# Performance work log

Measured on AMD Instinct MI355X. Metric: run time of the kernel, lower is better.

The kernel has to match this reference:

```python
import jax, jax.numpy as jnp
import numpy as np

N, E, G, H = 4096, 8192, 64, 128  # nodes, edges, graphs, hidden dim
NODE_DIM, EDGE_DIM = 11, 5


def _linear_params(key, fan_in, fan_out):
    kw, kb = jax.random.split(key)
    s = 1.0 / np.sqrt(fan_in)
    w = jax.random.uniform(kw, (fan_in, fan_out), minval=-s, maxval=s, dtype=jnp.float32)
    b = jax.random.uniform(kb, (fan_out,), minval=-s, maxval=s, dtype=jnp.float32)
    return w, b


def setup_inputs() -> dict:
    key = jax.random.key(0)
    ks = jax.random.split(key, 10)
    x = jax.random.normal(ks[0], (N, NODE_DIM), dtype=jnp.float32)
    edge_attr = jax.random.normal(ks[1], (E, EDGE_DIM), dtype=jnp.float32)
    edge_index = jax.random.randint(ks[2], (2, E), 0, N, dtype=jnp.int64)
    batch = jnp.sort(jax.random.randint(ks[3], (N,), 0, G, dtype=jnp.int64))
    # preprocess MLP: node_dim -> 128 -> 128
    p1_w, p1_b = _linear_params(ks[4], NODE_DIM, H)
    p2_w, p2_b = _linear_params(ks[5], H, H)
    # edge net: edge_dim -> 128 -> 256 -> 128 -> 128*128 (ReLU between, none after last)
    e1_w, e1_b = _linear_params(ks[6], EDGE_DIM, 128)
    e2_w, e2_b = _linear_params(ks[7], 128, 256)
    e3_w, e3_b = _linear_params(ks[8], 256, 128)
    e4_w, e4_b = _linear_params(ks[9], 128, H * H)
    return {"x": x, "edge_attr": edge_attr, "edge_index": edge_index, "batch": batch,
            "p1_w": p1_w, "p1_b": p1_b, "p2_w": p2_w, "p2_b": p2_b,
            "e1_w": e1_w, "e1_b": e1_b, "e2_w": e2_w, "e2_b": e2_b,
            "e3_w": e3_w, "e3_b": e3_b, "e4_w": e4_w, "e4_b": e4_b}


def reference(x, edge_attr, edge_index, batch,
              p1_w, p1_b, p2_w, p2_b,
              e1_w, e1_b, e2_w, e2_b, e3_w, e3_b, e4_w, e4_b):
    # node preprocess MLP (maps 11-dim features to 128 so NNConv dims are consistent)
    h = jax.nn.relu(x @ p1_w + p1_b) @ p2_w + p2_b  # [N, H]
    # edge network -> per-edge weight matrix [E, H, H]
    e = jax.nn.relu(edge_attr @ e1_w + e1_b)
    e = jax.nn.relu(e @ e2_w + e2_b)
    e = jax.nn.relu(e @ e3_w + e3_b)
    W = (e @ e4_w + e4_b).reshape(E, H, H)
    # NNConv (root_weight=False, bias=False, aggr='mean'):
    src, dst = edge_index[0], edge_index[1]
    msg = jnp.einsum('ei,eio->eo', h[src], W)  # gather + per-edge matmul, [E, H]
    agg = jax.ops.segment_sum(msg, dst, num_segments=N)
    cnt = jax.ops.segment_sum(jnp.ones((E,), msg.dtype), dst, num_segments=N)
    h_out = agg / jnp.maximum(cnt, 1.0)[:, None]  # scatter-mean, [N, H]
    # global add pool over graphs
    pooled = jax.ops.segment_sum(h_out, batch, num_segments=G)  # [G, H]
    return pooled
```

## Files before the change

kernel.cpp:

```cpp
#include <hip/hip_runtime.h>
#include <hip/hip_bf16.h>

#define N_NODES 4096
#define N_EDGES 8192
#define N_GRAPHS 64
#define HDIM 128

typedef __attribute__((ext_vector_type(8))) short bf16x8;
typedef __attribute__((ext_vector_type(4))) float f32x4;
typedef __attribute__((ext_vector_type(4))) unsigned short u16x4;

static __device__ __forceinline__ unsigned short f2bf(float f) {
    unsigned u = __builtin_bit_cast(unsigned, f);
    u += 0x7fffu + ((u >> 16) & 1u);
    return (unsigned short)(u >> 16);
}
static __device__ __forceinline__ float bf2f(unsigned short s) {
    unsigned u = ((unsigned)s) << 16;
    return __builtin_bit_cast(float, u);
}

__global__ __launch_bounds__(256) void fused_pre_kernel(
    const float* __restrict__ x, const float* __restrict__ p1w, const float* __restrict__ p1b,
    const float* __restrict__ p2w, const float* __restrict__ p2b, const float* __restrict__ e4b,
    unsigned short* __restrict__ h_bf, float* __restrict__ hb,
    const float* __restrict__ ea, const float* __restrict__ w1, const float* __restrict__ b1,
    const float* __restrict__ w2, const float* __restrict__ b2,
    const float* __restrict__ w3, const float* __restrict__ b3,
    unsigned short* __restrict__ e3bf,
    const float* __restrict__ w4, unsigned short* __restrict__ w4perm)
{
    __shared__ __align__(16) char smem[33024];
    const int t = threadIdx.x;
    const int bid = blockIdx.x;

    if (bid < 512) {
        float (*es)[5]   = (float(*)[5])smem;
        float (*l1t)[16] = (float(*)[16])(smem + 320);
        float (*l2t)[16] = (float(*)[16])(smem + 8512);
        const int eb = bid * 16;

        for (int r = t; r < 80; r += 256) es[r / 5][r % 5] = ea[(eb + r / 5) * 5 + r % 5];
        __syncthreads();
        {
            int j = t & 127;
            float wd[5];
            #pragma unroll
            for (int d = 0; d < 5; ++d) wd[d] = w1[d * 128 + j];
            float bj = b1[j];
            for (int p = 0; p < 8; ++p) {
                int e = p * 2 + (t >> 7);
                float acc = bj;
                #pragma unroll
                for (int d = 0; d < 5; ++d) acc += es[e][d] * wd[d];
                l1t[j][e] = fmaxf(acc, 0.f);
            }
        }
        __syncthreads();
        {
            float acc[16];
            float bj = b2[t];
            #pragma unroll
            for (int r = 0; r < 16; ++r) acc[r] = bj;
            for (int k = 0; k < 128; ++k) {
                float w = w2[k * 256 + t];
                const float4* row = (const float4*)&l1t[k][0];
                float4 v0 = row[0], v1 = row[1], v2 = row[2], v3 = row[3];
                acc[0]  += v0.x * w; acc[1]  += v0.y * w; acc[2]  += v0.z * w; acc[3]  += v0.w * w;
                acc[4]  += v1.x * w; acc[5]  += v1.y * w; acc[6]  += v1.z * w; acc[7]  += v1.w * w;
                acc[8]  += v2.x * w; acc[9]  += v2.y * w; acc[10] += v2.z * w; acc[11] += v2.w * w;
                acc[12] += v3.x * w; acc[13] += v3.y * w; acc[14] += v3.z * w; acc[15] += v3.w * w;
            }
            #pragma unroll
            for (int r = 0; r < 16; ++r) l2t[t][r] = fmaxf(acc[r], 0.f);
        }
        __syncthreads();
        {
            int j = t & 127, eh = t >> 7;
            float acc[8];
            float bj = b3[j];
            #pragma unroll
            for (int r = 0; r < 8; ++r) acc[r] = bj;
            for (int k = 0; k < 256; ++k) {
                float w = w3[k * 128 + j];
                const float4* row = (const float4*)&l2t[k][eh * 8];
                float4 v0 = row[0], v1 = row[1];
                acc[0] += v0.x * w; acc[1] += v0.y * w; acc[2] += v0.z * w; acc[3] += v0.w * w;
                acc[4] += v1.x * w; acc[5] += v1.y * w; acc[6] += v1.z * w; acc[7] += v1.w * w;
            }
            #pragma unroll
            for (int r = 0; r < 8; ++r)
                e3bf[(eb + eh * 8 + r) * 128 + j] = f2bf(fmaxf(acc[r], 0.f));
        }
    } else if (bid < 768) {
        float (*xs)[11]  = (float(*)[11])smem;
        float (*l1t)[16] = (float(*)[16])(smem + 704);
        float (*hs)[16]  = (float(*)[16])(smem + 8896);
        const int nb = bid - 512;

        for (int r = t; r < 16 * 11; r += 256) {
            int e = r / 11, d = r % 11;
            xs[e][d] = x[(nb * 16 + e) * 11 + d];
        }
        __syncthreads();
        {
            int j = t & 127;
            float wd[11];
            #pragma unroll
            for (int d = 0; d < 11; ++d) wd[d] = p1w[d * 128 + j];
            float bj = p1b[j];
            for (int p = 0; p < 8; ++p) {
                int e = p * 2 + (t >> 7);
                float acc = bj;
                #pragma unroll
                for (int d = 0; d < 11; ++d) acc += xs[e][d] * wd[d];
                l1t[j][e] = fmaxf(acc, 0.f);
            }
        }
        __syncthreads();
        {
            int j = t & 127, eh = t >> 7;
            float acc[8];
            float bj = p2b[j];
            #pragma unroll
            for (int r = 0; r < 8; ++r) acc[r] = bj;
            for (int k = 0; k < 128; ++k) {
                float w = p2w[k * 128 + j];
                const float4* row = (const float4*)&l1t[k][eh * 8];
                float4 v0 = row[0], v1 = row[1];
                acc[0] += v0.x * w; acc[1] += v0.y * w; acc[2] += v0.z * w; acc[3] += v0.w * w;
                acc[4] += v1.x * w; acc[5] += v1.y * w; acc[6] += v1.z * w; acc[7] += v1.w * w;
            }
            #pragma unroll
            for (int r = 0; r < 8; ++r) {
                int e = eh * 8 + r;
                h_bf[(nb * 16 + e) * 128 + j] = f2bf(acc[r]);
                hs[j][e] = acc[r];
            }
        }
        __syncthreads();
        {
            int j = t & 127, eh = t >> 7;
            float acc[8] = {0.f,0.f,0.f,0.f,0.f,0.f,0.f,0.f};
            for (int i = 0; i < 128; ++i) {
                float w = e4b[i * 128 + j];
                const float4* row = (const float4*)&hs[i][eh * 8];
                float4 v0 = row[0], v1 = row[1];
                acc[0] += v0.x * w; acc[1] += v0.y * w; acc[2] += v0.z * w; acc[3] += v0.w * w;
                acc[4] += v1.x * w; acc[5] += v1.y * w; acc[6] += v1.z * w; acc[7] += v1.w * w;
            }
            #pragma unroll
            for (int r = 0; r < 8; ++r) hb[(nb * 16 + eh * 8 + r) * 128 + j] = acc[r];
        }
    } else {
        unsigned short (*tt)[129] = (unsigned short(*)[129])smem;
        const int i = bid - 768;
        for (int r = t; r < 16384; r += 256) {
            int k = r >> 7, o = r & 127;
            tt[o][k] = f2bf(w4[k * 16384 + i * 128 + o]);
        }
        __syncthreads();
        for (int r = t; r < 16384; r += 256) {
            int o = r >> 7, k = r & 127;
            w4perm[((size_t)(o >> 5) * 128 + i) * 4352 + (size_t)(o & 31) * 136 + k] = tt[o][k];
        }
    }
}

__global__ __launch_bounds__(256, 2) void nnconv_kernel(
    const unsigned short* __restrict__ e3bf, const unsigned short* __restrict__ h_bf,
    const unsigned short* __restrict__ w4perm, const float* __restrict__ hb,
    const int* __restrict__ ei, float* __restrict__ agg, float* __restrict__ cnt)
{
    __shared__ __align__(16) unsigned short ldsB[17408];
    __shared__ __align__(16) unsigned short ht_t[16384];
    const int t = threadIdx.x;
    const int bid = blockIdx.x;
    const int xcd    = bid & 7;
    const int osplit = xcd >> 1;
    const int ksplit = xcd & 1;
    const int etile  = bid >> 3;
    const int w = t >> 6, lane = t & 63, q = lane >> 4, l15 = lane & 15;
    const int mg = w >> 1;
    const int og = w & 1;
    const int e0 = etile * 128;
    const int o0 = osplit * 32;
    const int k0 = ksplit * 64;

    auto stage = [&](int buf, int gi) {
        const char* src = (const char*)w4perm + ((size_t)osplit * 128 + gi) * 8704;
        char* dst = (char*)ldsB + buf * 17408;
        #pragma unroll
        for (int it = 0; it < 4; ++it) {
            int off = it * 4096 + t * 16;
            __builtin_amdgcn_global_load_lds(
                (const __attribute__((address_space(1))) unsigned int*)(src + off),
                (__attribute__((address_space(3))) unsigned int*)(dst + off), 16, 0, 0);
        }
        if (t < 64) {
            int off = 16384 + t * 16;
            __builtin_amdgcn_global_load_lds(
                (const __attribute__((address_space(1))) unsigned int*)(src + off),
                (__attribute__((address_space(3))) unsigned int*)(dst + off), 16, 0, 0);
        }
    };

    stage(0, k0);

    bf16x8 afrag[4][4];
    #pragma unroll
    for (int mb = 0; mb < 4; ++mb)
        #pragma unroll
        for (int s = 0; s < 4; ++s) {
            int row = e0 + mg * 64 + mb * 16 + l15;
            afrag[mb][s] = *(const bf16x8*)(e3bf + row * 128 + s * 32 + q * 8);
        }

    {
        int r = t >> 1, part = t & 1;
        int s = ei[e0 + r];
        #pragma unroll
        for (int u = 0; u < 8; ++u) {
            uint4 v = *(const uint4*)(h_bf + (size_t)s * 128 + part * 64 + u * 8);
            const unsigned short* pv = (const unsigned short*)&v;
            #pragma unroll
            for (int j = 0; j < 8; ++j) ht_t[(part * 64 + u * 8 + j) * 128 + r] = pv[j];
        }
    }

    f32x4 acc[4];
    #pragma unroll
    for (int mb = 0; mb < 4; ++mb) acc[mb] = (f32x4){0.f, 0.f, 0.f, 0.f};
    const f32x4 zero4 = (f32x4){0.f, 0.f, 0.f, 0.f};

    __syncthreads();

    auto compute = [&](int bufbase , int gi) {
        float hv[4][4];
        #pragma unroll
        for (int mb = 0; mb < 4; ++mb) {
            u16x4 hr = *(const u16x4*)&ht_t[gi * 128 + mg * 64 + mb * 16 + q * 4];
            #pragma unroll
            for (int r = 0; r < 4; ++r) hv[mb][r] = bf2f(hr[r]);
        }
        bf16x8 bfrag[4];
        #pragma unroll
        for (int s = 0; s < 4; ++s)
            bfrag[s] = *(const bf16x8*)&ldsB[bufbase + (og * 16 + l15) * 136 + s * 32 + q * 8];
        #pragma unroll
        for (int mb = 0; mb < 4; ++mb) {
            f32x4 tmp = __builtin_amdgcn_mfma_f32_16x16x32_bf16(afrag[mb][0], bfrag[0], zero4, 0, 0, 0);
            tmp = __builtin_amdgcn_mfma_f32_16x16x32_bf16(afrag[mb][1], bfrag[1], tmp, 0, 0, 0);
            tmp = __builtin_amdgcn_mfma_f32_16x16x32_bf16(afrag[mb][2], bfrag[2], tmp, 0, 0, 0);
            tmp = __builtin_amdgcn_mfma_f32_16x16x32_bf16(afrag[mb][3], bfrag[3], tmp, 0, 0, 0);
            #pragma unroll
            for (int r = 0; r < 4; ++r)
                acc[mb][r] += hv[mb][r] * tmp[r];
        }
    };

    int buf = 0;
    for (int p = 0; p < 32; ++p) {
        if (p + 1 < 32) stage(buf ^ 1, k0 + 2 * p + 2);
        compute(buf * 8704,        k0 + 2 * p);
        compute(buf * 8704 + 4352, k0 + 2 * p + 1);
        if (p + 1 < 32) __syncthreads();
        buf ^= 1;
    }

    #pragma unroll
    for (int mb = 0; mb < 4; ++mb) {
        #pragma unroll
        for (int r = 0; r < 4; ++r) {
            int e = e0 + mg * 64 + mb * 16 + q * 4 + r;
            int de = ei[N_EDGES + e];
            int se = ei[e];
            if (xcd == 0 && og == 0 && l15 == 0) atomicAdd(&cnt[de], 1.0f);
            int o = o0 + og * 16 + l15;
            float v = acc[mb][r];
            if (ksplit == 0) v += hb[(size_t)se * 128 + o];
            atomicAdd(&agg[(size_t)de * 128 + o], v);
        }
    }
}

__global__ __launch_bounds__(128) void pool_kernel(
    const float* __restrict__ agg, const float* __restrict__ cnt,
    const int* __restrict__ batch, float* __restrict__ out)
{
    const int g = blockIdx.x, t = threadIdx.x;
    int lo = 0, hi = N_NODES;
    while (lo < hi) { int m = (lo + hi) >> 1; if (batch[m] < g) lo = m + 1; else hi = m; }
    const int n_lo = lo;
    int lo2 = n_lo, hi2 = N_NODES;
    while (lo2 < hi2) { int m = (lo2 + hi2) >> 1; if (batch[m] < g + 1) lo2 = m + 1; else hi2 = m; }
    const int n_hi = lo2;

    float s0 = 0.f, s1 = 0.f, s2 = 0.f, s3 = 0.f;
    int n = n_lo;
    for (; n + 4 <= n_hi; n += 4) {
        float c0 = cnt[n], c1 = cnt[n + 1], c2 = cnt[n + 2], c3 = cnt[n + 3];
        float v0 = agg[(n    ) * 128 + t];
        float v1 = agg[(n + 1) * 128 + t];
        float v2 = agg[(n + 2) * 128 + t];
        float v3 = agg[(n + 3) * 128 + t];
        s0 += v0 / (c0 > 1.f ? c0 : 1.f);
        s1 += v1 / (c1 > 1.f ? c1 : 1.f);
        s2 += v2 / (c2 > 1.f ? c2 : 1.f);
        s3 += v3 / (c3 > 1.f ? c3 : 1.f);
    }
    for (; n < n_hi; ++n) {
        float c = cnt[n];
        s0 += agg[n * 128 + t] / (c > 1.f ? c : 1.f);
    }
    out[g * 128 + t] = (s0 + s1) + (s2 + s3);
}

extern "C" void kernel_launch(void* const* d_in, const int* in_sizes, int n_in,
                              void* d_out, int out_size, void* d_ws, size_t ws_size,
                              hipStream_t stream)
{
    const float* x     = (const float*)d_in[0];
    const float* ea    = (const float*)d_in[1];
    const int*   ei    = (const int*)d_in[2];
    const int*   batch = (const int*)d_in[3];
    const float* p1w   = (const float*)d_in[4];
    const float* p1b   = (const float*)d_in[5];
    const float* p2w   = (const float*)d_in[6];
    const float* p2b   = (const float*)d_in[7];
    const float* w1    = (const float*)d_in[8];
    const float* b1    = (const float*)d_in[9];
    const float* w2    = (const float*)d_in[10];
    const float* b2    = (const float*)d_in[11];
    const float* w3    = (const float*)d_in[12];
    const float* b3    = (const float*)d_in[13];
    const float* w4    = (const float*)d_in[14];
    const float* b4    = (const float*)d_in[15];
    float* out = (float*)d_out;
    (void)in_sizes; (void)n_in; (void)out_size; (void)ws_size;

    char* ws = (char*)d_ws;
    unsigned short* h_bf = (unsigned short*)(ws);
    unsigned short* e3bf = (unsigned short*)(ws + 1048576);
    float* hb            = (float*)(ws + 3145728);
    unsigned short* w4p  = (unsigned short*)(ws + 5242880);
    float* agg           = (float*)(ws + 9699328);
    float* cnt           = (float*)(ws + 11796480);

    hipMemsetAsync(agg, 0, (size_t)N_NODES * 128 * 4 + (size_t)N_NODES * 4, stream);

    fused_pre_kernel<<<896, 256, 0, stream>>>(
        x, p1w, p1b, p2w, p2b, b4, h_bf, hb,
        ea, w1, b1, w2, b2, w3, b3, e3bf,
        w4, w4p);
    nnconv_kernel<<<512, 256, 0, stream>>>(e3bf, h_bf, w4p, hb, ei, agg, cnt);
    pool_kernel<<<N_GRAPHS, 128, 0, stream>>>(agg, cnt, batch, out);
}
```

Baseline: 183.0 us.

## Read edge-net weight fragments directly from global, drop LDS staging pipeline

Removes the double-buffered global-to-LDS staging of the permuted W4 slices and the per-iteration barriers; each wave now loads its B fragments straight from global memory (relying on cache reuse across waves). The gathered source-node features are stored in LDS as fp32 and only for this block's half of the input dimension, shrinking LDS use, and the launch bound is raised to three blocks per CU. This trades explicit prefetch and LDS sharing of weights for fewer barriers and higher occupancy, at the risk of exposed global-load latency and redundant fragment loads across waves.

```diff
diff --git a/kernel.cpp b/kernel.cpp
--- a/kernel.cpp
+++ b/kernel.cpp
@@ -167,13 +167,12 @@
     }
 }
 
-__global__ __launch_bounds__(256, 2) void nnconv_kernel(
+__global__ __launch_bounds__(256, 3) void nnconv_kernel(
     const unsigned short* __restrict__ e3bf, const unsigned short* __restrict__ h_bf,
     const unsigned short* __restrict__ w4perm, const float* __restrict__ hb,
     const int* __restrict__ ei, float* __restrict__ agg, float* __restrict__ cnt)
 {
-    __shared__ __align__(16) unsigned short ldsB[17408];
-    __shared__ __align__(16) unsigned short ht_t[16384];
+    __shared__ __align__(16) float ht_f[64 * 128];
     const int t = threadIdx.x;
     const int bid = blockIdx.x;
     const int xcd    = bid & 7;
@@ -185,27 +184,7 @@
     const int og = w & 1;
     const int e0 = etile * 128;
     const int o0 = osplit * 32;
-    const int k0 = ksplit * 64;
-
-    auto stage = [&](int buf, int gi) {
-        const char* src = (const char*)w4perm + ((size_t)osplit * 128 + gi) * 8704;
-        char* dst = (char*)ldsB + buf * 17408;
-        #pragma unroll
-        for (int it = 0; it < 4; ++it) {
-            int off = it * 4096 + t * 16;
-            __builtin_amdgcn_global_load_lds(
-                (const __attribute__((address_space(1))) unsigned int*)(src + off),
-                (__attribute__((address_space(3))) unsigned int*)(dst + off), 16, 0, 0);
-        }
-        if (t < 64) {
-            int off = 16384 + t * 16;
-            __builtin_amdgcn_global_load_lds(
-                (const __attribute__((address_space(1))) unsigned int*)(src + off),
-                (__attribute__((address_space(3))) unsigned int*)(dst + off), 16, 0, 0);
-        }
-    };
-
-    stage(0, k0);
+    const int i0 = ksplit * 64;
 
     bf16x8 afrag[4][4];
     #pragma unroll
@@ -220,11 +199,12 @@
         int r = t >> 1, part = t & 1;
         int s = ei[e0 + r];
         #pragma unroll
-        for (int u = 0; u < 8; ++u) {
-            uint4 v = *(const uint4*)(h_bf + (size_t)s * 128 + part * 64 + u * 8);
+        for (int u = 0; u < 4; ++u) {
+            uint4 v = *(const uint4*)(h_bf + (size_t)s * 128 + i0 + part * 32 + u * 8);
             const unsigned short* pv = (const unsigned short*)&v;
             #pragma unroll
-            for (int j = 0; j < 8; ++j) ht_t[(part * 64 + u * 8 + j) * 128 + r] = pv[j];
+            for (int j = 0; j < 8; ++j)
+                ht_f[(part * 32 + u * 8 + j) * 128 + r] = bf2f(pv[j]);
         }
     }
 
@@ -235,37 +215,26 @@
 
     __syncthreads();
 
-    auto compute = [&](int bufbase , int gi) {
-        float hv[4][4];
+    const unsigned short* bbase =
+        w4perm + (size_t)(osplit * 128 + i0) * 4352 + (og * 16 + l15) * 136 + q * 8;
+    #pragma unroll 2
+    for (int c = 0; c < 64; ++c) {
+        const unsigned short* bp = bbase + (size_t)c * 4352;
+        bf16x8 bfrag[4];
+        #pragma unroll
+        for (int s = 0; s < 4; ++s)
+            bfrag[s] = *(const bf16x8*)(bp + s * 32);
         #pragma unroll
         for (int mb = 0; mb < 4; ++mb) {
-            u16x4 hr = *(const u16x4*)&ht_t[gi * 128 + mg * 64 + mb * 16 + q * 4];
-            #pragma unroll
-            for (int r = 0; r < 4; ++r) hv[mb][r] = bf2f(hr[r]);
-        }
-        bf16x8 bfrag[4];
-        #pragma unroll
-        for (int s = 0; s < 4; ++s)
-            bfrag[s] = *(const bf16x8*)&ldsB[bufbase + (og * 16 + l15) * 136 + s * 32 + q * 8];
-        #pragma unroll
-        for (int mb = 0; mb < 4; ++mb) {
+            f32x4 hv = *(const f32x4*)&ht_f[c * 128 + mg * 64 + mb * 16 + q * 4];
             f32x4 tmp = __builtin_amdgcn_mfma_f32_16x16x32_bf16(afrag[mb][0], bfrag[0], zero4, 0, 0, 0);
             tmp = __builtin_amdgcn_mfma_f32_16x16x32_bf16(afrag[mb][1], bfrag[1], tmp, 0, 0, 0);
             tmp = __builtin_amdgcn_mfma_f32_16x16x32_bf16(afrag[mb][2], bfrag[2], tmp, 0, 0, 0);
             tmp = __builtin_amdgcn_mfma_f32_16x16x32_bf16(afrag[mb][3], bfrag[3], tmp, 0, 0, 0);
             #pragma unroll
             for (int r = 0; r < 4; ++r)
-                acc[mb][r] += hv[mb][r] * tmp[r];
-        }
-    };
-
-    int buf = 0;
-    for (int p = 0; p < 32; ++p) {
-        if (p + 1 < 32) stage(buf ^ 1, k0 + 2 * p + 2);
-        compute(buf * 8704,        k0 + 2 * p);
-        compute(buf * 8704 + 4352, k0 + 2 * p + 1);
-        if (p + 1 < 32) __syncthreads();
-        buf ^= 1;
+                acc[mb][r] += hv[r] * tmp[r];
+        }
     }
 
     #pragma unroll
```

Result: no change. 183.9 us (+0.5%).
